# Kernel tuning notes

Hardware: AMD Instinct MI355X
Metric: run time of the kernel (lower is better)

The kernel has to match this reference:

```python
import jax, jax.numpy as jnp
import numpy as np

B, S, D, N, C = 32, 1024, 256, 32, 64
ROUTING_ITERS = 3


def setup_inputs() -> dict:
    key = jax.random.key(0)
    k1, k2 = jax.random.split(key)
    x = jax.random.normal(k1, (B, S, D), dtype=jnp.float32)
    W = jax.random.normal(k2, (N, D, C), dtype=jnp.float32) * 0.1
    return {"x": x, "W": W}


def _squash(s, eps=1e-8):
    # s: [B, N, C]; squash along last dim
    sq_norm = jnp.sum(s * s, axis=-1, keepdims=True)
    return (sq_norm / (1.0 + sq_norm)) * s / jnp.sqrt(sq_norm + eps)


def reference(x, W):
    # Prediction vectors: u_hat[b,s,n,c] = sum_d x[b,s,d] * W[n,d,c]
    u_hat = jnp.einsum('bsd,ndc->bsnc', x, W)  # [B, S, N, C]
    b_logits = jnp.zeros(u_hat.shape[:3], dtype=u_hat.dtype)  # [B, S, N]
    v = None
    for i in range(ROUTING_ITERS):
        c = jax.nn.softmax(b_logits, axis=2)               # [B, S, N]
        s = jnp.einsum('bsn,bsnc->bnc', c, u_hat)          # [B, N, C]
        v = _squash(s)                                      # [B, N, C]
        if i < ROUTING_ITERS - 1:
            agreement = jnp.einsum('bsnc,bnc->bsn', u_hat, v)
            b_logits = b_logits + agreement
    return v
```

## Files before the change

kernel.cpp:

```cpp
#include <hip/hip_runtime.h>
#include <math.h>

namespace {
constexpr int B_ = 32, S_ = 1024, D_ = 256, N_ = 32, C_ = 64;
constexpr int NC_ = N_ * C_;
constexpr int CHUNKS_ = 16;
constexpr int SCHUNK_ = 64;
constexpr int XP_ = 16;

typedef __bf16 bf16x8 __attribute__((ext_vector_type(8)));
typedef __bf16 bf16x4 __attribute__((ext_vector_type(4)));
typedef float floatx4 __attribute__((ext_vector_type(4)));

constexpr int XS_ = 264;
constexpr int TS_ = 264;
constexpr int CS_ = 72;
}

extern "C" __global__ __launch_bounds__(256) void k_xsum(
    const float* __restrict__ x, float* __restrict__ xsum_part) {
  const int b = blockIdx.x, sb = blockIdx.y, t = threadIdx.x;
  const float* xb = x + ((size_t)b * S_ + sb * 64) * D_;
  float a = 0.f;
  #pragma unroll 8
  for (int s = 0; s < 64; ++s) a += xb[s * D_ + t];
  xsum_part[((size_t)b * XP_ + sb) * D_ + t] = a;
}

extern "C" __global__ __launch_bounds__(256) void k_small(
    const float* __restrict__ z, const float* __restrict__ W,
    float* __restrict__ t_fp, __bf16* __restrict__ t_bhi,
    __bf16* __restrict__ t_blo, float* __restrict__ vout,
    int P, int zb, int zp, int zn, float scale, int accum, int final_) {
  __shared__ float zloc[256];
  __shared__ float sq_red[4][64];
  __shared__ float v_lds[64];
  const int b = blockIdx.x, n = blockIdx.y, t = threadIdx.x;

  float a = 0.f;
  for (int p = 0; p < P; ++p) a += z[(size_t)b * zb + (size_t)p * zp + n * zn + t];
  zloc[t] = a;
  __syncthreads();

  const int c = t & 63, dq = t >> 6;
  const float* Wn = W + (size_t)n * (D_ * C_);
  float s = 0.f;
  #pragma unroll 8
  for (int dd = 0; dd < 64; ++dd) {
    int d = dq * 64 + dd;
    s += zloc[d] * Wn[d * 64 + c];
  }
  sq_red[dq][c] = s;
  __syncthreads();

  if (t < 64) {
    float sc = (sq_red[0][t] + sq_red[1][t] + sq_red[2][t] + sq_red[3][t]) * scale;
    float sq = sc * sc;
    #pragma unroll
    for (int m = 1; m <= 32; m <<= 1) sq += __shfl_xor(sq, m);
    float scl = sq / ((1.f + sq) * sqrtf(sq + 1e-8f));
    float v = sc * scl;
    v_lds[t] = v;
    if (final_) vout[(size_t)b * NC_ + n * 64 + t] = v;
  }
  __syncthreads();

  if (!final_) {
    const float4* W4 = (const float4*)W + (size_t)n * 4096 + t * 16;
    float acc = 0.f;
    #pragma unroll
    for (int q = 0; q < 16; ++q) {
      float4 wv = W4[q];
      acc += wv.x * v_lds[q * 4] + wv.y * v_lds[q * 4 + 1] +
             wv.z * v_lds[q * 4 + 2] + wv.w * v_lds[q * 4 + 3];
    }
    size_t idx = ((size_t)b * N_ + n) * D_ + t;
    float tf = acc + (accum ? t_fp[idx] : 0.f);
    t_fp[idx] = tf;
    __bf16 hi = (__bf16)tf;
    t_bhi[idx] = hi;
    t_blo[idx] = (__bf16)(tf - (float)hi);
  }
}

extern "C" __global__ __launch_bounds__(256) void k_pass(
    const float* __restrict__ x, const __bf16* __restrict__ t_bhi,
    const __bf16* __restrict__ t_blo, float* __restrict__ p_part) {
  __shared__ __align__(16) __bf16 x_lds[SCHUNK_ * XS_];
  __shared__ __align__(16) __bf16 th_lds[N_ * TS_];
  __shared__ __align__(16) __bf16 tl_lds[N_ * TS_];
  __shared__ __align__(16) __bf16 c_Th[N_ * CS_];
  __shared__ __align__(16) __bf16 c_Tl[N_ * CS_];
  const int b = blockIdx.x, ch = blockIdx.y;
  const int t = threadIdx.x, w = t >> 6, lane = t & 63;
  const int quad = lane >> 4, l16 = lane & 15;

  #pragma unroll
  for (int e = 0; e < 4; ++e) {
    int idx = e * 2048 + t * 8;
    int n = idx >> 8, d = idx & 255;
    *(uint4*)(th_lds + n * TS_ + d) = *(const uint4*)(t_bhi + (size_t)b * 8192 + idx);
    *(uint4*)(tl_lds + n * TS_ + d) = *(const uint4*)(t_blo + (size_t)b * 8192 + idx);
  }
  const float* xb = x + ((size_t)b * S_ + ch * SCHUNK_) * D_;
  #pragma unroll
  for (int i = 0; i < 16; ++i) {
    int pos = i * 1024 + t * 4;
    int row = pos >> 8, col = pos & 255;
    float4 f = *(const float4*)(xb + row * D_ + col);
    bf16x4 p4;
    p4[0] = (__bf16)f.x; p4[1] = (__bf16)f.y; p4[2] = (__bf16)f.z; p4[3] = (__bf16)f.w;
    *(bf16x4*)(x_lds + row * XS_ + col) = p4;
  }
  __syncthreads();

  floatx4 acc[2];
  acc[0] = (floatx4){0.f, 0.f, 0.f, 0.f};
  acc[1] = (floatx4){0.f, 0.f, 0.f, 0.f};
  const int sbase = w * 16;
  #pragma unroll
  for (int k0 = 0; k0 < 256; k0 += 32) {
    int ks = k0 + quad * 8;
    bf16x8 bfrag = *(const bf16x8*)(x_lds + (sbase + l16) * XS_ + ks);
    #pragma unroll
    for (int i = 0; i < 2; ++i) {
      bf16x8 ah = *(const bf16x8*)(th_lds + (i * 16 + l16) * TS_ + ks);
      bf16x8 al = *(const bf16x8*)(tl_lds + (i * 16 + l16) * TS_ + ks);
      acc[i] = __builtin_amdgcn_mfma_f32_16x16x32_bf16(ah, bfrag, acc[i], 0, 0, 0);
      acc[i] = __builtin_amdgcn_mfma_f32_16x16x32_bf16(al, bfrag, acc[i], 0, 0, 0);
    }
  }
  float mx = -1e30f;
  #pragma unroll
  for (int i = 0; i < 2; ++i)
    #pragma unroll
    for (int r = 0; r < 4; ++r) mx = fmaxf(mx, acc[i][r]);
  mx = fmaxf(mx, __shfl_xor(mx, 16));
  mx = fmaxf(mx, __shfl_xor(mx, 32));
  float e_[2][4];
  float ss = 0.f;
  #pragma unroll
  for (int i = 0; i < 2; ++i)
    #pragma unroll
    for (int r = 0; r < 4; ++r) { e_[i][r] = __expf(acc[i][r] - mx); ss += e_[i][r]; }
  ss += __shfl_xor(ss, 16);
  ss += __shfl_xor(ss, 32);
  float inv = 1.f / ss;
  #pragma unroll
  for (int i = 0; i < 2; ++i)
    #pragma unroll
    for (int r = 0; r < 4; ++r) {
      float cv = e_[i][r] * inv;
      __bf16 chi = (__bf16)cv;
      int o = (i * 16 + quad * 4 + r) * CS_ + sbase + l16;
      c_Th[o] = chi;
      c_Tl[o] = (__bf16)(cv - (float)chi);
    }
  __syncthreads();

  floatx4 acc2[2][4];
  #pragma unroll
  for (int i = 0; i < 2; ++i)
    #pragma unroll
    for (int dt = 0; dt < 4; ++dt) acc2[i][dt] = (floatx4){0.f, 0.f, 0.f, 0.f};
  const int dbase = w * 64;
  #pragma unroll
  for (int k0 = 0; k0 < 64; k0 += 32) {
    int ks = k0 + quad * 8;
    bf16x8 ah[2], al[2];
    #pragma unroll
    for (int i = 0; i < 2; ++i) {
      ah[i] = *(const bf16x8*)(c_Th + (i * 16 + l16) * CS_ + ks);
      al[i] = *(const bf16x8*)(c_Tl + (i * 16 + l16) * CS_ + ks);
    }
    #pragma unroll
    for (int dt = 0; dt < 4; ++dt) {
      bf16x8 bb;
      #pragma unroll
      for (int j8 = 0; j8 < 8; ++j8)
        bb[j8] = x_lds[(ks + j8) * XS_ + dbase + dt * 16 + l16];
      #pragma unroll
      for (int i = 0; i < 2; ++i) {
        acc2[i][dt] = __builtin_amdgcn_mfma_f32_16x16x32_bf16(ah[i], bb, acc2[i][dt], 0, 0, 0);
        acc2[i][dt] = __builtin_amdgcn_mfma_f32_16x16x32_bf16(al[i], bb, acc2[i][dt], 0, 0, 0);
      }
    }
  }
  float* pp = p_part + ((size_t)b * CHUNKS_ + ch) * (N_ * D_);
  #pragma unroll
  for (int i = 0; i < 2; ++i)
    #pragma unroll
    for (int dt = 0; dt < 4; ++dt)
      #pragma unroll
      for (int r = 0; r < 4; ++r) {
        int n = i * 16 + quad * 4 + r;
        int d = dbase + dt * 16 + l16;
        pp[n * D_ + d] = acc2[i][dt][r];
      }
}

extern "C" void kernel_launch(void* const* d_in, const int* in_sizes, int n_in,
                              void* d_out, int out_size, void* d_ws, size_t ws_size,
                              hipStream_t stream) {
  const float* x = (const float*)d_in[0];
  const float* W = (const float*)d_in[1];
  float* out = (float*)d_out;

  char* ws = (char*)d_ws;
  float* xsum_part = (float*)ws;
  float* p_part = xsum_part + B_ * XP_ * D_;
  float* t_fp = p_part + (size_t)B_ * CHUNKS_ * N_ * D_;
  __bf16* t_bhi = (__bf16*)(t_fp + B_ * N_ * D_);
  __bf16* t_blo = t_bhi + B_ * N_ * D_;

  k_xsum<<<dim3(B_, XP_), 256, 0, stream>>>(x, xsum_part);
  k_small<<<dim3(B_, N_), 256, 0, stream>>>(
      xsum_part, W, t_fp, t_bhi, t_blo, nullptr,
      XP_, XP_ * D_, D_, 0, 1.f / 32.f, 0, 0);

  k_pass<<<dim3(B_, CHUNKS_), 256, 0, stream>>>(x, t_bhi, t_blo, p_part);
  k_small<<<dim3(B_, N_), 256, 0, stream>>>(
      p_part, W, t_fp, t_bhi, t_blo, nullptr,
      CHUNKS_, CHUNKS_ * N_ * D_, N_ * D_, D_, 1.f, 1, 0);

  k_pass<<<dim3(B_, CHUNKS_), 256, 0, stream>>>(x, t_bhi, t_blo, p_part);
  k_small<<<dim3(B_, N_), 256, 0, stream>>>(
      p_part, W, t_fp, t_bhi, t_blo, out,
      CHUNKS_, CHUNKS_ * N_ * D_, N_ * D_, D_, 1.f, 0, 1);
}
```

Measured before the change: 160.6 us.

## Pre-convert x to bf16 once and atomically accumulate pass partials

The first staging kernel now also writes a bf16 copy of x to workspace, so each routing pass reads half the bytes instead of re-reading and converting fp32 x. The per-chunk partial buffers are replaced by atomicAdd into a per-batch accumulator, which the preceding small kernel zeroes. The small kernels then read one summed buffer instead of reducing 16 partials. This adds a 16 MB bf16 write and atomic contention on the output in exchange.

```diff
diff --git a/kernel.cpp b/kernel.cpp
--- a/kernel.cpp
+++ b/kernel.cpp
@@ -4,8 +4,6 @@
 namespace {
 constexpr int B_ = 32, S_ = 1024, D_ = 256, N_ = 32, C_ = 64;
 constexpr int NC_ = N_ * C_;
-constexpr int CHUNKS_ = 16;
-constexpr int SCHUNK_ = 64;
 constexpr int XP_ = 16;
 
 typedef __bf16 bf16x8 __attribute__((ext_vector_type(8)));
@@ -17,20 +15,33 @@
 constexpr int CS_ = 72;
 }
 
-extern "C" __global__ __launch_bounds__(256) void k_xsum(
-    const float* __restrict__ x, float* __restrict__ xsum_part) {
+extern "C" __global__ __launch_bounds__(256) void k_stage(
+    const float* __restrict__ x, float* __restrict__ xsum_part,
+    __bf16* __restrict__ xb_ws) {
   const int b = blockIdx.x, sb = blockIdx.y, t = threadIdx.x;
   const float* xb = x + ((size_t)b * S_ + sb * 64) * D_;
   float a = 0.f;
   #pragma unroll 8
   for (int s = 0; s < 64; ++s) a += xb[s * D_ + t];
   xsum_part[((size_t)b * XP_ + sb) * D_ + t] = a;
+
+  __bf16* xo = xb_ws + ((size_t)(b * XP_ + sb)) * (64 * D_);
+  #pragma unroll
+  for (int i = 0; i < 16; ++i) {
+    int pos = i * 1024 + t * 4;
+    float4 f = *(const float4*)(xb + pos);
+    bf16x4 p4;
+    p4[0] = (__bf16)f.x; p4[1] = (__bf16)f.y;
+    p4[2] = (__bf16)f.z; p4[3] = (__bf16)f.w;
+    *(bf16x4*)(xo + pos) = p4;
+  }
 }
 
 extern "C" __global__ __launch_bounds__(256) void k_small(
     const float* __restrict__ z, const float* __restrict__ W,
     float* __restrict__ t_fp, __bf16* __restrict__ t_bhi,
     __bf16* __restrict__ t_blo, float* __restrict__ vout,
+    float* __restrict__ yzero,
     int P, int zb, int zp, int zn, float scale, int accum, int final_) {
   __shared__ float zloc[256];
   __shared__ float sq_red[4][64];
@@ -40,6 +51,7 @@
   float a = 0.f;
   for (int p = 0; p < P; ++p) a += z[(size_t)b * zb + (size_t)p * zp + n * zn + t];
   zloc[t] = a;
+  if (yzero) yzero[((size_t)b * N_ + n) * D_ + t] = 0.f;
   __syncthreads();
 
   const int c = t & 63, dq = t >> 6;
@@ -66,7 +78,7 @@
   __syncthreads();
 
   if (!final_) {
-    const float4* W4 = (const float4*)W + (size_t)n * 4096 + t * 16;
+    const float4* W4 = (const float4*)Wn + t * 16;
     float acc = 0.f;
     #pragma unroll
     for (int q = 0; q < 16; ++q) {
@@ -84,9 +96,9 @@
 }
 
 extern "C" __global__ __launch_bounds__(256) void k_pass(
-    const float* __restrict__ x, const __bf16* __restrict__ t_bhi,
-    const __bf16* __restrict__ t_blo, float* __restrict__ p_part) {
-  __shared__ __align__(16) __bf16 x_lds[SCHUNK_ * XS_];
+    const __bf16* __restrict__ xb_ws, const __bf16* __restrict__ t_bhi,
+    const __bf16* __restrict__ t_blo, float* __restrict__ y) {
+  __shared__ __align__(16) __bf16 x_lds[64 * XS_];
   __shared__ __align__(16) __bf16 th_lds[N_ * TS_];
   __shared__ __align__(16) __bf16 tl_lds[N_ * TS_];
   __shared__ __align__(16) __bf16 c_Th[N_ * CS_];
@@ -102,15 +114,12 @@
     *(uint4*)(th_lds + n * TS_ + d) = *(const uint4*)(t_bhi + (size_t)b * 8192 + idx);
     *(uint4*)(tl_lds + n * TS_ + d) = *(const uint4*)(t_blo + (size_t)b * 8192 + idx);
   }
-  const float* xb = x + ((size_t)b * S_ + ch * SCHUNK_) * D_;
-  #pragma unroll
-  for (int i = 0; i < 16; ++i) {
-    int pos = i * 1024 + t * 4;
-    int row = pos >> 8, col = pos & 255;
-    float4 f = *(const float4*)(xb + row * D_ + col);
-    bf16x4 p4;
-    p4[0] = (__bf16)f.x; p4[1] = (__bf16)f.y; p4[2] = (__bf16)f.z; p4[3] = (__bf16)f.w;
-    *(bf16x4*)(x_lds + row * XS_ + col) = p4;
+  const __bf16* xsrc = xb_ws + ((size_t)(b * XP_ + ch)) * (64 * D_);
+  #pragma unroll
+  for (int e = 0; e < 8; ++e) {
+    int idx = e * 2048 + t * 8;
+    int row = idx >> 8, col = idx & 255;
+    *(uint4*)(x_lds + row * XS_ + col) = *(const uint4*)(xsrc + idx);
   }
   __syncthreads();
 
@@ -175,18 +184,17 @@
     }
     #pragma unroll
     for (int dt = 0; dt < 4; ++dt) {
-      bf16x8 bb;
+      bf16x8 bfr;
       #pragma unroll
       for (int j8 = 0; j8 < 8; ++j8)
-        bb[j8] = x_lds[(ks + j8) * XS_ + dbase + dt * 16 + l16];
+        bfr[j8] = x_lds[(ks + j8) * XS_ + dbase + dt * 16 + l16];
       #pragma unroll
       for (int i = 0; i < 2; ++i) {
-        acc2[i][dt] = __builtin_amdgcn_mfma_f32_16x16x32_bf16(ah[i], bb, acc2[i][dt], 0, 0, 0);
-        acc2[i][dt] = __builtin_amdgcn_mfma_f32_16x16x32_bf16(al[i], bb, acc2[i][dt], 0, 0, 0);
+        acc2[i][dt] = __builtin_amdgcn_mfma_f32_16x16x32_bf16(ah[i], bfr, acc2[i][dt], 0, 0, 0);
+        acc2[i][dt] = __builtin_amdgcn_mfma_f32_16x16x32_bf16(al[i], bfr, acc2[i][dt], 0, 0, 0);
       }
     }
   }
-  float* pp = p_part + ((size_t)b * CHUNKS_ + ch) * (N_ * D_);
   #pragma unroll
   for (int i = 0; i < 2; ++i)
     #pragma unroll
@@ -195,7 +203,7 @@
       for (int r = 0; r < 4; ++r) {
         int n = i * 16 + quad * 4 + r;
         int d = dbase + dt * 16 + l16;
-        pp[n * D_ + d] = acc2[i][dt][r];
+        atomicAdd(&y[((size_t)b * N_ + n) * D_ + d], acc2[i][dt][r]);
       }
 }
 
@@ -207,24 +215,29 @@
   float* out = (float*)d_out;
 
   char* ws = (char*)d_ws;
-  float* xsum_part = (float*)ws;
-  float* p_part = xsum_part + B_ * XP_ * D_;
-  float* t_fp = p_part + (size_t)B_ * CHUNKS_ * N_ * D_;
+  __bf16* xb_ws = (__bf16*)ws;
+  float* xsum_part = (float*)(ws + 16777216);
+  float* y1 = (float*)(ws + 16777216 + 524288);
+  float* y2 = y1 + B_ * N_ * D_;
+  float* t_fp = y2 + B_ * N_ * D_;
   __bf16* t_bhi = (__bf16*)(t_fp + B_ * N_ * D_);
   __bf16* t_blo = t_bhi + B_ * N_ * D_;
 
-  k_xsum<<<dim3(B_, XP_), 256, 0, stream>>>(x, xsum_part);
+  k_stage<<<dim3(B_, XP_), 256, 0, stream>>>(x, xsum_part, xb_ws);
+
   k_small<<<dim3(B_, N_), 256, 0, stream>>>(
-      xsum_part, W, t_fp, t_bhi, t_blo, nullptr,
+      xsum_part, W, t_fp, t_bhi, t_blo, nullptr, y1,
       XP_, XP_ * D_, D_, 0, 1.f / 32.f, 0, 0);
 
-  k_pass<<<dim3(B_, CHUNKS_), 256, 0, stream>>>(x, t_bhi, t_blo, p_part);
+  k_pass<<<dim3(B_, XP_), 256, 0, stream>>>(xb_ws, t_bhi, t_blo, y1);
+
   k_small<<<dim3(B_, N_), 256, 0, stream>>>(
-      p_part, W, t_fp, t_bhi, t_blo, nullptr,
-      CHUNKS_, CHUNKS_ * N_ * D_, N_ * D_, D_, 1.f, 1, 0);
-
-  k_pass<<<dim3(B_, CHUNKS_), 256, 0, stream>>>(x, t_bhi, t_blo, p_part);
+      y1, W, t_fp, t_bhi, t_blo, nullptr, y2,
+      1, N_ * D_, 0, D_, 1.f, 1, 0);
+
+  k_pass<<<dim3(B_, XP_), 256, 0, stream>>>(xb_ws, t_bhi, t_blo, y2);
+
   k_small<<<dim3(B_, N_), 256, 0, stream>>>(
-      p_part, W, t_fp, t_bhi, t_blo, out,
-      CHUNKS_, CHUNKS_ * N_ * D_, N_ * D_, D_, 1.f, 0, 1);
-}
+      y2, W, t_fp, t_bhi, t_blo, out, nullptr,
+      1, N_ * D_, 0, D_, 1.f, 0, 1);
+}
```

Result: no change. 157.9 us (-1.7%).
